# Optimization experiments

Hardware: AMD Instinct MI355X
Metric: run time of the kernel (lower is better)

## Reference

```python
import jax, jax.numpy as jnp
import numpy as np

N, E, F, C, ED, G, D = 50000, 1000000, 30, 64, 11, 1024, 256


def setup_inputs() -> dict:
    key = jax.random.key(0)
    ks = jax.random.split(key, 20)
    rn = lambda k, shape, s=0.1: jax.random.normal(k, shape, jnp.float32) * s
    return {
        "x": rn(ks[0], (N, F), 1.0),
        "edge_attr": jax.random.uniform(ks[1], (E, ED), jnp.float32),
        "W0": rn(ks[2], (F, C)), "asrc0": rn(ks[3], (C,)), "adst0": rn(ks[4], (C,)),
        "We0": rn(ks[5], (ED, C)), "ae0": rn(ks[6], (C,)), "Wres0": rn(ks[7], (F, C)),
        "b0": jnp.zeros((C,), jnp.float32),
        "W": rn(ks[8], (3, C, C)), "asrc": rn(ks[9], (3, C)), "adst": rn(ks[10], (3, C)),
        "We": rn(ks[11], (3, ED, C)), "ae": rn(ks[12], (3, C)), "Wres": rn(ks[13], (3, C, C)),
        "b": jnp.zeros((3, C), jnp.float32),
        "Wout": rn(ks[14], (2 * C, D)), "bout": jnp.zeros((D,), jnp.float32),
        "edge_index": jax.random.randint(ks[15], (2, E), 0, N),
        "batch_index": jnp.sort(jax.random.randint(ks[16], (N,), 0, G)),
    }


def _gat(x, src, dst, edge_attr, W, asrc, adst, We, ae, Wres, b):
    """PyG GATConv (heads=1) with edge_dim and residual=True."""
    n = x.shape[0]
    h = x @ W                                   # [N, C]
    e = edge_attr @ We                          # [E, C]
    alpha = (jnp.sum(h * asrc, -1)[src]
             + jnp.sum(h * adst, -1)[dst]
             + jnp.sum(e * ae, -1))             # [E]
    alpha = jax.nn.leaky_relu(alpha, 0.2)
    m = jax.ops.segment_max(alpha, dst, num_segments=n)
    a = jnp.exp(alpha - m[dst])
    s = jax.ops.segment_sum(a, dst, num_segments=n)
    a = a / (s[dst] + 1e-16)                    # per-dst softmax
    out = jax.ops.segment_sum(a[:, None] * h[src], dst, num_segments=n)
    return out + x @ Wres + b


def reference(x, edge_attr, W0, asrc0, adst0, We0, ae0, Wres0, b0,
              W, asrc, adst, We, ae, Wres, b, Wout, bout,
              edge_index, batch_index):
    src, dst = edge_index[0], edge_index[1]
    h = jax.nn.leaky_relu(
        _gat(x, src, dst, edge_attr, W0, asrc0, adst0, We0, ae0, Wres0, b0), 0.01)
    for i in range(3):  # conv1..conv3 (fixed small layer loop)
        h = _gat(h, src, dst, edge_attr, W[i], asrc[i], adst[i],
                 We[i], ae[i], Wres[i], b[i])
        if i < 2:
            h = jax.nn.leaky_relu(h, 0.01)
    gmax = jax.ops.segment_max(h, batch_index, num_segments=G)
    gmax = jnp.where(jnp.isfinite(gmax), gmax, 0.0)  # empty graphs -> 0
    cnt = jax.ops.segment_sum(jnp.ones((h.shape[0],), h.dtype), batch_index,
                              num_segments=G)
    gmean = jax.ops.segment_sum(h, batch_index, num_segments=G) / jnp.maximum(cnt, 1.0)[:, None]
    pooled = jax.nn.leaky_relu(jnp.concatenate([gmax, gmean], axis=1), 0.01)
    return pooled @ Wout + bout
```

## Files before the change

kernel.cpp:

```cpp
#include <hip/hip_runtime.h>
#include <hip/hip_fp16.h>

#define NN 50000
#define NE 1000000
#define FIN0 30
#define C 64
#define ED 11
#define NG 1024
#define DOUT 256
#define NBIN 196
#define PA_EDGES 2048

typedef unsigned long long ull;

__global__ __launch_bounds__(256) void hist196_kernel(const int* __restrict__ dst,
    int* __restrict__ bcnt){
  __shared__ int h[256];
  int t=threadIdx.x;
  h[t]=0;
  __syncthreads();
  for(int i=blockIdx.x*256+t;i<NE;i+=gridDim.x*256)
    atomicAdd(&h[dst[i]>>8],1);
  __syncthreads();
  if(h[t]) atomicAdd(&bcnt[t],h[t]);
}

__global__ __launch_bounds__(256) void scan196_kernel(const int* __restrict__ bcnt,
    int* __restrict__ bbase, int* __restrict__ gcur){
  __shared__ int p[256];
  int t=threadIdx.x;
  int v=bcnt[t];
  p[t]=v; __syncthreads();
  #pragma unroll
  for(int off=1;off<256;off<<=1){
    int u=(t>=off)?p[t-off]:0;
    __syncthreads(); p[t]+=u; __syncthreads();
  }
  int ex=p[t]-v;
  if(t<=NBIN) bbase[t]=ex;
  if(t<NBIN)  gcur[t]=ex;
}

__global__ __launch_bounds__(256) void grow_kernel(const int* __restrict__ batch,
    int* __restrict__ growptr){
  int i=blockIdx.x*256+threadIdx.x;
  if(i>=NN) return;
  int bi=batch[i];
  int bp=(i==0)?-1:batch[i-1];
  for(int g=bp+1;g<=bi;++g) growptr[g]=i;
  if(i==NN-1){ for(int g=bi+1;g<=NG;++g) growptr[g]=NN; }
}

__global__ __launch_bounds__(256) void part_kernel(const int* __restrict__ dst,
    const int* __restrict__ src, const float* __restrict__ edge_attr,
    const float* __restrict__ We0, const float* __restrict__ ae0,
    const float* __restrict__ We,  const float* __restrict__ ae,
    int* __restrict__ gcur, uint4* __restrict__ prec){
  __shared__ uint4 lrec[PA_EDGES];
  __shared__ unsigned char lbin[PA_EDGES];
  __shared__ float tile[256*ED];
  __shared__ float sw[4][ED];
  __shared__ int hist[256], p[256], sc[256], lofs[256], bb[256];
  int t=threadIdx.x;
  hist[t]=0;
  if(t<4*ED){
    int l=t/ED, j=t%ED;
    const float* wp=(l==0)? (We0+(size_t)j*C) : (We+((size_t)(l-1)*ED+j)*C);
    const float* ap=(l==0)? ae0 : (ae+(size_t)(l-1)*C);
    float s=0.f;
    for(int c=0;c<C;++c) s+=wp[c]*ap[c];
    sw[l][j]=s;
  }
  __syncthreads();
  size_t e0=(size_t)blockIdx.x*PA_EDGES;
  int cnt=(int)min((size_t)PA_EDGES,(size_t)NE-e0);
  for(int i=t;i<cnt;i+=256) atomicAdd(&hist[dst[e0+i]>>8],1);
  __syncthreads();
  p[t]=hist[t]; __syncthreads();
  #pragma unroll
  for(int off=1;off<256;off<<=1){
    int u=(t>=off)?p[t-off]:0;
    __syncthreads(); p[t]+=u; __syncthreads();
  }
  sc[t]=p[t]-hist[t];
  lofs[t]=sc[t];
  bb[t]=(hist[t]>0)?atomicAdd(&gcur[t],hist[t]):0;
  __syncthreads();
  for(int base=0;base<cnt;base+=256){
    int ccnt=min(256,cnt-base);
    for(int i=t;i<ccnt*ED;i+=256) tile[i]=edge_attr[(e0+base)*ED+i];
    __syncthreads();
    if(t<ccnt){
      int i=base+t;
      int d=dst[e0+i], s=src[e0+i];
      int b=d>>8;
      float d0=0,d1=0,d2=0,d3=0;
      #pragma unroll
      for(int j=0;j<ED;++j){
        float ev=tile[t*ED+j];
        d0=fmaf(ev,sw[0][j],d0);
        d1=fmaf(ev,sw[1][j],d1);
        d2=fmaf(ev,sw[2][j],d2);
        d3=fmaf(ev,sw[3][j],d3);
      }
      uint4 r;
      r.x=(unsigned)d; r.y=(unsigned)s;
      r.z=(unsigned)__half_as_ushort(__float2half(d0))
         |((unsigned)__half_as_ushort(__float2half(d1))<<16);
      r.w=(unsigned)__half_as_ushort(__float2half(d2))
         |((unsigned)__half_as_ushort(__float2half(d3))<<16);
      int slot=atomicAdd(&lofs[b],1);
      lrec[slot]=r;
      lbin[slot]=(unsigned char)b;
    }
    __syncthreads();
  }
  for(int i=t;i<cnt;i+=256){
    int b=lbin[i];
    int g=bb[b]+i-sc[b];
    prec[g]=lrec[i];
  }
}

__global__ __launch_bounds__(256) void build_kernel(const uint4* __restrict__ prec,
    const int* __restrict__ bbase,
    int* __restrict__ rowptr, int* __restrict__ src_csr, ushort* __restrict__ edch){
  __shared__ int cnt[256], p[256], cur[256];
  int t=threadIdx.x, b=blockIdx.x;
  int n0=b<<8;
  cnt[t]=0;
  __syncthreads();
  int beg=bbase[b], endd=bbase[b+1];
  for(int j=beg+t;j<endd;j+=256)
    atomicAdd(&cnt[(int)prec[j].x-n0],1);
  __syncthreads();
  int v=cnt[t];
  p[t]=v; __syncthreads();
  #pragma unroll
  for(int off=1;off<256;off<<=1){
    int u=(t>=off)?p[t-off]:0;
    __syncthreads(); p[t]+=u; __syncthreads();
  }
  int ex=p[t]-v;
  cur[t]=beg+ex;
  if(n0+t<NN) rowptr[n0+t]=beg+ex;
  if(b==0&&t==0) rowptr[NN]=NE;
  __syncthreads();
  for(int j=beg+t;j<endd;j+=256){
    uint4 r=prec[j];
    int d=(int)r.x, s=(int)r.y;
    int pos=atomicAdd(&cur[d-n0],1);
    src_csr[pos]=s;
    edch[pos]                =(ushort)(r.z&0xffffu);
    edch[(size_t)NE+pos]     =(ushort)(r.z>>16);
    edch[2*(size_t)NE+pos]   =(ushort)(r.w&0xffffu);
    edch[3*(size_t)NE+pos]   =(ushort)(r.w>>16);
  }
}

template<int FIN, int SXS>
__global__ __launch_bounds__(256) void feat_kernel(const float* __restrict__ in,
    const float* __restrict__ W, const float* __restrict__ Wres,
    const float* __restrict__ bvec, const float* __restrict__ av_src,
    const float* __restrict__ av_dst,
    __half* __restrict__ hW16, float* __restrict__ outb,
    float* __restrict__ as_, float* __restrict__ ad_){
  __shared__ float sW[FIN*C], sR[FIN*C];
  __shared__ float sx[64*SXS];
  __shared__ float sb[C], ss[C], sd[C];
  int tid=threadIdx.x;
  if(tid<C){ sb[tid]=bvec[tid]; ss[tid]=av_src[tid]; sd[tid]=av_dst[tid]; }
  for(int i=tid;i<FIN*C;i+=256){ sW[i]=W[i]; sR[i]=Wres[i]; }
  int nbase=blockIdx.x*64;
  int nvalid=min(64,NN-nbase);
  if constexpr (FIN==64){
    const float4* in4=(const float4*)(in+(size_t)nbase*64);
    for(int i=tid;i<1024;i+=256){
      int n=i>>4, k=(i&15)*4;
      float4 v=(n<nvalid)?in4[i]:make_float4(0.f,0.f,0.f,0.f);
      *(float4*)&sx[n*SXS+k]=v;
    }
  } else {
    for(int i=tid;i<64*FIN;i+=256){
      int n=i/FIN, k=i-n*FIN;
      sx[n*SXS+k]=(n<nvalid)?in[(size_t)(nbase+n)*FIN+k]:0.f;
    }
  }
  __syncthreads();
  int w=tid>>6, lane=tid&63;
  int ng=lane>>4, cl=lane&15;
  int n0=w*16+ng*4;
  int c0=cl*4;
  float hw[4][4]={}, hr[4][4]={};
  const float* sxp=&sx[n0*SXS];
  #pragma unroll 2
  for(int k=0;k<FIN;k+=2){
    float4 wv0=*(const float4*)&sW[k*C+c0];
    float4 rv0=*(const float4*)&sR[k*C+c0];
    float4 wv1=*(const float4*)&sW[(k+1)*C+c0];
    float4 rv1=*(const float4*)&sR[(k+1)*C+c0];
    float2 x0=*(const float2*)&sxp[k];
    float2 x1=*(const float2*)&sxp[SXS+k];
    float2 x2=*(const float2*)&sxp[2*SXS+k];
    float2 x3=*(const float2*)&sxp[3*SXS+k];
    float xa[4]={x0.x,x1.x,x2.x,x3.x};
    float xb[4]={x0.y,x1.y,x2.y,x3.y};
    #pragma unroll
    for(int r=0;r<4;++r){
      hw[r][0]=fmaf(xa[r],wv0.x,hw[r][0]);
      hw[r][1]=fmaf(xa[r],wv0.y,hw[r][1]);
      hw[r][2]=fmaf(xa[r],wv0.z,hw[r][2]);
      hw[r][3]=fmaf(xa[r],wv0.w,hw[r][3]);
      hr[r][0]=fmaf(xa[r],rv0.x,hr[r][0]);
      hr[r][1]=fmaf(xa[r],rv0.y,hr[r][1]);
      hr[r][2]=fmaf(xa[r],rv0.z,hr[r][2]);
      hr[r][3]=fmaf(xa[r],rv0.w,hr[r][3]);
      hw[r][0]=fmaf(xb[r],wv1.x,hw[r][0]);
      hw[r][1]=fmaf(xb[r],wv1.y,hw[r][1]);
      hw[r][2]=fmaf(xb[r],wv1.z,hw[r][2]);
      hw[r][3]=fmaf(xb[r],wv1.w,hw[r][3]);
      hr[r][0]=fmaf(xb[r],rv1.x,hr[r][0]);
      hr[r][1]=fmaf(xb[r],rv1.y,hr[r][1]);
      hr[r][2]=fmaf(xb[r],rv1.z,hr[r][2]);
      hr[r][3]=fmaf(xb[r],rv1.w,hr[r][3]);
    }
  }
  float s0=ss[c0], s1=ss[c0+1], s2=ss[c0+2], s3=ss[c0+3];
  float d0=sd[c0], d1=sd[c0+1], d2=sd[c0+2], d3=sd[c0+3];
  float b0v=sb[c0], b1v=sb[c0+1], b2v=sb[c0+2], b3v=sb[c0+3];
  #pragma unroll
  for(int r=0;r<4;++r){
    int n=n0+r;
    float ps=hw[r][0]*s0+hw[r][1]*s1+hw[r][2]*s2+hw[r][3]*s3;
    float pd=hw[r][0]*d0+hw[r][1]*d1+hw[r][2]*d2+hw[r][3]*d3;
    #pragma unroll
    for(int off=1;off<16;off<<=1){ ps+=__shfl_xor(ps,off,64); pd+=__shfl_xor(pd,off,64); }
    if(n<nvalid){
      size_t gn=(size_t)(nbase+n);
      ushort4 hv;
      hv.x=__half_as_ushort(__float2half(hw[r][0]));
      hv.y=__half_as_ushort(__float2half(hw[r][1]));
      hv.z=__half_as_ushort(__float2half(hw[r][2]));
      hv.w=__half_as_ushort(__float2half(hw[r][3]));
      *(ushort4*)&hW16[gn*C+c0]=hv;
      float4 ov;
      ov.x=hr[r][0]+b0v; ov.y=hr[r][1]+b1v; ov.z=hr[r][2]+b2v; ov.w=hr[r][3]+b3v;
      *(float4*)&outb[gn*C+c0]=ov;
      if(cl==0){ as_[gn]=ps; ad_[gn]=pd; }
    }
  }
}

__device__ __forceinline__ void acc8(float* a, float at, uint4 u){
  __half2 h0=*(__half2*)&u.x, h1=*(__half2*)&u.y, h2=*(__half2*)&u.z, h3=*(__half2*)&u.w;
  float2 f0=__half22float2(h0), f1=__half22float2(h1);
  float2 f2=__half22float2(h2), f3=__half22float2(h3);
  a[0]=fmaf(at,f0.x,a[0]); a[1]=fmaf(at,f0.y,a[1]);
  a[2]=fmaf(at,f1.x,a[2]); a[3]=fmaf(at,f1.y,a[3]);
  a[4]=fmaf(at,f2.x,a[4]); a[5]=fmaf(at,f2.y,a[5]);
  a[6]=fmaf(at,f3.x,a[6]); a[7]=fmaf(at,f3.y,a[7]);
}

__global__ __launch_bounds__(256) void agg_kernel(const int* __restrict__ rowptr,
    const int* __restrict__ src_csr, const ushort* __restrict__ edc_l,
    const float* __restrict__ as_, const float* __restrict__ ad_,
    const __half* __restrict__ hW16, float* __restrict__ outb, int relu){
  __shared__ float2 sws[4][64];
  int w=threadIdx.x>>6, lane=threadIdx.x&63;
  int half=lane>>5, hl=lane&31;
  int n0=blockIdx.x*8+w*2;
  int nidx=n0+half;
  int beg=rowptr[nidx], end=rowptr[nidx+1];
  int deg=end-beg;
  const uint4* hw4=(const uint4*)hW16;

  if(__all(deg<=32)){
    float ad_n=ad_[nidx];
    int j=beg+hl;
    float al=-INFINITY; int sl=0;
    if(hl<deg){
      sl=src_csr[j];
      float a=as_[sl]+ad_n+__half2float(__ushort_as_half(edc_l[j]));
      al=(a>0.f)?a:0.2f*a;
    }
    float mn=al;
    #pragma unroll
    for(int off=16;off;off>>=1) mn=fmaxf(mn,__shfl_xor(mn,off,64));
    float wl=(hl<deg)?__expf(al-mn):0.f;
    float s=wl;
    #pragma unroll
    for(int off=16;off;off>>=1) s+=__shfl_xor(s,off,64);
    float2 pr; pr.x=wl; pr.y=__int_as_float(sl);
    sws[w][lane]=pr;
    int g=hl>>3, gl=hl&7;
    float acc[8]={0.f,0.f,0.f,0.f,0.f,0.f,0.f,0.f};
    int base=half*32;
    int t=g;
    for(; t+4<deg; t+=8){
      float2 r0=sws[w][base+t], r1=sws[w][base+t+4];
      uint4 u0=hw4[(size_t)__float_as_int(r0.y)*8+gl];
      uint4 u1=hw4[(size_t)__float_as_int(r1.y)*8+gl];
      acc8(acc,r0.x,u0);
      acc8(acc,r1.x,u1);
    }
    if(t<deg){
      float2 r=sws[w][base+t];
      uint4 u=hw4[(size_t)__float_as_int(r.y)*8+gl];
      acc8(acc,r.x,u);
    }
    #pragma unroll
    for(int off=8;off<=16;off<<=1){
      #pragma unroll
      for(int i=0;i<8;++i) acc[i]+=__shfl_xor(acc[i],off,64);
    }
    if(hl<8){
      float denom=s+1e-16f;
      size_t o0=(size_t)nidx*C+hl*8;
      float4 oa=*(float4*)&outb[o0];
      float4 ob=*(float4*)&outb[o0+4];
      float4 va,vb;
      va.x=acc[0]/denom+oa.x; va.y=acc[1]/denom+oa.y;
      va.z=acc[2]/denom+oa.z; va.w=acc[3]/denom+oa.w;
      vb.x=acc[4]/denom+ob.x; vb.y=acc[5]/denom+ob.y;
      vb.z=acc[6]/denom+ob.z; vb.w=acc[7]/denom+ob.w;
      if(relu){
        va.x=(va.x>0.f)?va.x:0.01f*va.x; va.y=(va.y>0.f)?va.y:0.01f*va.y;
        va.z=(va.z>0.f)?va.z:0.01f*va.z; va.w=(va.w>0.f)?va.w:0.01f*va.w;
        vb.x=(vb.x>0.f)?vb.x:0.01f*vb.x; vb.y=(vb.y>0.f)?vb.y:0.01f*vb.y;
        vb.z=(vb.z>0.f)?vb.z:0.01f*vb.z; vb.w=(vb.w>0.f)?vb.w:0.01f*vb.w;
      }
      *(float4*)&outb[o0]=va;
      *(float4*)&outb[o0+4]=vb;
    }
    return;
  }

  for(int h=0;h<2;++h){
    int m=n0+h;
    int bh=__shfl(beg,h*32,64);
    int dh=__shfl(deg,h*32,64);
    float ad_n=ad_[m];
    int g2=lane>>3, gl2=lane&7;
    float s=0.f;
    float acc[8]={0.f,0.f,0.f,0.f,0.f,0.f,0.f,0.f};
    if(dh<=64){
      int j=bh+lane;
      float al=-INFINITY; int sl=0;
      if(lane<dh){
        sl=src_csr[j];
        float a=as_[sl]+ad_n+__half2float(__ushort_as_half(edc_l[j]));
        al=(a>0.f)?a:0.2f*a;
      }
      float mn=al;
      #pragma unroll
      for(int off=32;off;off>>=1) mn=fmaxf(mn,__shfl_xor(mn,off,64));
      float wl=(lane<dh)?__expf(al-mn):0.f;
      s=wl;
      #pragma unroll
      for(int off=32;off;off>>=1) s+=__shfl_xor(s,off,64);
      float2 pr; pr.x=wl; pr.y=__int_as_float(sl);
      sws[w][lane]=pr;
      int t=g2;
      for(; t+8<dh; t+=16){
        float2 r0=sws[w][t], r1=sws[w][t+8];
        uint4 u0=hw4[(size_t)__float_as_int(r0.y)*8+gl2];
        uint4 u1=hw4[(size_t)__float_as_int(r1.y)*8+gl2];
        acc8(acc,r0.x,u0);
        acc8(acc,r1.x,u1);
      }
      if(t<dh){
        float2 r=sws[w][t];
        uint4 u=hw4[(size_t)__float_as_int(r.y)*8+gl2];
        acc8(acc,r.x,u);
      }
    } else {
      float m_=-INFINITY;
      for(int base=bh;base<bh+dh;base+=64){
        int j=base+lane;
        float al=-INFINITY; int sl=0;
        if(j<bh+dh){
          sl=src_csr[j];
          float a=as_[sl]+ad_n+__half2float(__ushort_as_half(edc_l[j]));
          al=(a>0.f)?a:0.2f*a;
        }
        float cm=al;
        #pragma unroll
        for(int off=32;off;off>>=1) cm=fmaxf(cm,__shfl_xor(cm,off,64));
        float mn=fmaxf(m_,cm);
        float scale=(m_==-INFINITY)?0.f:__expf(m_-mn);
        s*=scale;
        #pragma unroll
        for(int i=0;i<8;++i) acc[i]*=scale;
        float wl=(j<bh+dh)?__expf(al-mn):0.f;
        float cs=wl;
        #pragma unroll
        for(int off=32;off;off>>=1) cs+=__shfl_xor(cs,off,64);
        s+=cs; m_=mn;
        float2 pr; pr.x=wl; pr.y=__int_as_float(sl);
        sws[w][lane]=pr;
        int cnt=min(64,bh+dh-base);
        int t=g2;
        for(; t+8<cnt; t+=16){
          float2 r0=sws[w][t], r1=sws[w][t+8];
          uint4 u0=hw4[(size_t)__float_as_int(r0.y)*8+gl2];
          uint4 u1=hw4[(size_t)__float_as_int(r1.y)*8+gl2];
          acc8(acc,r0.x,u0);
          acc8(acc,r1.x,u1);
        }
        if(t<cnt){
          float2 r=sws[w][t];
          uint4 u=hw4[(size_t)__float_as_int(r.y)*8+gl2];
          acc8(acc,r.x,u);
        }
      }
    }
    #pragma unroll
    for(int off=8;off<64;off<<=1){
      #pragma unroll
      for(int i=0;i<8;++i) acc[i]+=__shfl_xor(acc[i],off,64);
    }
    if(g2==0){
      float denom=s+1e-16f;
      size_t o0=(size_t)m*C+gl2*8;
      float4 oa=*(float4*)&outb[o0];
      float4 ob=*(float4*)&outb[o0+4];
      float4 va,vb;
      va.x=acc[0]/denom+oa.x; va.y=acc[1]/denom+oa.y;
      va.z=acc[2]/denom+oa.z; va.w=acc[3]/denom+oa.w;
      vb.x=acc[4]/denom+ob.x; vb.y=acc[5]/denom+ob.y;
      vb.z=acc[6]/denom+ob.z; vb.w=acc[7]/denom+ob.w;
      if(relu){
        va.x=(va.x>0.f)?va.x:0.01f*va.x; va.y=(va.y>0.f)?va.y:0.01f*va.y;
        va.z=(va.z>0.f)?va.z:0.01f*va.z; va.w=(va.w>0.f)?va.w:0.01f*va.w;
        vb.x=(vb.x>0.f)?vb.x:0.01f*vb.x; vb.y=(vb.y>0.f)?vb.y:0.01f*vb.y;
        vb.z=(vb.z>0.f)?vb.z:0.01f*vb.z; vb.w=(vb.w>0.f)?vb.w:0.01f*vb.w;
      }
      *(float4*)&outb[o0]=va;
      *(float4*)&outb[o0+4]=vb;
    }
  }
}

__global__ __launch_bounds__(256) void pool_kernel(const float* __restrict__ h,
    const int* __restrict__ growptr, float* __restrict__ pooled){
  int w=threadIdx.x>>6, lane=threadIdx.x&63;
  int g=blockIdx.x*4+w;
  if(g>=NG) return;
  int beg=growptr[g], end=growptr[g+1];
  float mx=-INFINITY, sm=0.f;
  for(int n=beg;n<end;++n){ float v=h[(size_t)n*C+lane]; mx=fmaxf(mx,v); sm+=v; }
  int cnt=end-beg;
  float gm=(cnt==0)?0.f:mx;
  float mean=sm/fmaxf((float)cnt,1.f);
  gm=(gm>0.f)?gm:0.01f*gm;
  mean=(mean>0.f)?mean:0.01f*mean;
  pooled[(size_t)g*128+lane]=gm;
  pooled[(size_t)g*128+64+lane]=mean;
}

__global__ __launch_bounds__(256) void out_kernel(const float* __restrict__ pooled,
    const float* __restrict__ Wout, const float* __restrict__ bout,
    float* __restrict__ out){
  __shared__ float sp[128];
  int g=blockIdx.x, d=threadIdx.x;
  if(d<128) sp[d]=pooled[(size_t)g*128+d];
  __syncthreads();
  float o=bout[d];
  for(int k=0;k<128;++k) o=fmaf(sp[k],Wout[k*DOUT+d],o);
  out[(size_t)g*DOUT+d]=o;
}

extern "C" void kernel_launch(void* const* d_in, const int* in_sizes, int n_in,
                              void* d_out, int out_size, void* d_ws, size_t ws_size,
                              hipStream_t stream){
  const float* x        =(const float*)d_in[0];
  const float* edge_attr=(const float*)d_in[1];
  const float* W0       =(const float*)d_in[2];
  const float* asrc0    =(const float*)d_in[3];
  const float* adst0    =(const float*)d_in[4];
  const float* We0      =(const float*)d_in[5];
  const float* ae0      =(const float*)d_in[6];
  const float* Wres0    =(const float*)d_in[7];
  const float* b0       =(const float*)d_in[8];
  const float* W        =(const float*)d_in[9];
  const float* asrc     =(const float*)d_in[10];
  const float* adst     =(const float*)d_in[11];
  const float* We       =(const float*)d_in[12];
  const float* ae       =(const float*)d_in[13];
  const float* Wres     =(const float*)d_in[14];
  const float* b        =(const float*)d_in[15];
  const float* Wout     =(const float*)d_in[16];
  const float* bout     =(const float*)d_in[17];
  const int* edge_index =(const int*)d_in[18];
  const int* batch_index=(const int*)d_in[19];
  const int* src=edge_index;
  const int* dst=edge_index+NE;

  char* p=(char*)d_ws;
  auto take=[&](size_t bytes)->void*{ void* r=(void*)p; p+=(bytes+255)&~(size_t)255; return r; };
  int* rowptr  =(int*)take((size_t)(NN+1)*4);
  int* growptr =(int*)take((size_t)(NG+1)*4);
  int* bcnt    =(int*)take((size_t)256*4);
  int* bbase   =(int*)take((size_t)256*4);
  int* gcur    =(int*)take((size_t)256*4);
  int* src_csr =(int*)take((size_t)NE*4);
  float* as_   =(float*)take((size_t)NN*4);
  float* ad_   =(float*)take((size_t)NN*4);
  ushort* edch =(ushort*)take((size_t)NE*4*2);
  __half* hW16 =(__half*)take((size_t)NN*C*2);
  float* bufA  =(float*)take((size_t)NN*C*4);
  uint4* prec  =(uint4*)take((size_t)NE*16);
  float* bufB  =(float*)prec;
  float* pooled=(float*)take((size_t)NG*128*4);
  (void)ws_size; (void)in_sizes; (void)n_in; (void)out_size;

  hipMemsetAsync(bcnt,0,(size_t)256*4,stream);
  hist196_kernel<<<1024,256,0,stream>>>(dst,bcnt);
  scan196_kernel<<<1,256,0,stream>>>(bcnt,bbase,gcur);
  grow_kernel<<<(NN+255)/256,256,0,stream>>>(batch_index,growptr);

  part_kernel<<<(NE+PA_EDGES-1)/PA_EDGES,256,0,stream>>>(dst,src,edge_attr,
      We0,ae0,We,ae,gcur,prec);
  build_kernel<<<NBIN,256,0,stream>>>(prec,bbase,rowptr,src_csr,edch);

  const int nblkF=(NN+63)/64;
  const int nblkA=NN/8;
  feat_kernel<FIN0,36><<<nblkF,256,0,stream>>>(x,W0,Wres0,b0,asrc0,adst0,hW16,bufA,as_,ad_);
  agg_kernel<<<nblkA,256,0,stream>>>(rowptr,src_csr,edch,as_,ad_,hW16,bufA,1);
  float* bin=bufA; float* bo=bufB;
  for(int i=0;i<3;++i){
    feat_kernel<C,68><<<nblkF,256,0,stream>>>(bin,W+(size_t)i*C*C,Wres+(size_t)i*C*C,
        b+(size_t)i*C,asrc+(size_t)i*C,adst+(size_t)i*C,hW16,bo,as_,ad_);
    agg_kernel<<<nblkA,256,0,stream>>>(rowptr,src_csr,edch+(size_t)(i+1)*NE,as_,ad_,hW16,bo,(i<2)?1:0);
    float* t=bin; bin=bo; bo=t;
  }
  pool_kernel<<<(NG+3)/4,256,0,stream>>>(bin,growptr,pooled);
  out_kernel<<<NG,256,0,stream>>>(pooled,Wout,bout,(float*)d_out);
}
```

Measured before the change: 312.5 us.

## Shrink partition tiles, use wave-shuffle scan, and drop shared staging buffers

```diff
diff --git a/kernel.cpp b/kernel.cpp
--- a/kernel.cpp
+++ b/kernel.cpp
@@ -9,7 +9,7 @@
 #define NG 1024
 #define DOUT 256
 #define NBIN 196
-#define PA_EDGES 2048
+#define PA_EDGES 1024
 
 typedef unsigned long long ull;
 
@@ -57,10 +57,9 @@
     const float* __restrict__ We,  const float* __restrict__ ae,
     int* __restrict__ gcur, uint4* __restrict__ prec){
   __shared__ uint4 lrec[PA_EDGES];
-  __shared__ unsigned char lbin[PA_EDGES];
-  __shared__ float tile[256*ED];
   __shared__ float sw[4][ED];
-  __shared__ int hist[256], p[256], sc[256], lofs[256], bb[256];
+  __shared__ int hist[256], sc[256], lofs[256], bb[256];
+  __shared__ int wsum[4];
   int t=threadIdx.x;
   hist[t]=0;
   if(t<4*ED){
@@ -74,51 +73,64 @@
   __syncthreads();
   size_t e0=(size_t)blockIdx.x*PA_EDGES;
   int cnt=(int)min((size_t)PA_EDGES,(size_t)NE-e0);
-  for(int i=t;i<cnt;i+=256) atomicAdd(&hist[dst[e0+i]>>8],1);
-  __syncthreads();
-  p[t]=hist[t]; __syncthreads();
-  #pragma unroll
-  for(int off=1;off<256;off<<=1){
-    int u=(t>=off)?p[t-off]:0;
-    __syncthreads(); p[t]+=u; __syncthreads();
-  }
-  sc[t]=p[t]-hist[t];
-  lofs[t]=sc[t];
-  bb[t]=(hist[t]>0)?atomicAdd(&gcur[t],hist[t]):0;
-  __syncthreads();
-  for(int base=0;base<cnt;base+=256){
-    int ccnt=min(256,cnt-base);
-    for(int i=t;i<ccnt*ED;i+=256) tile[i]=edge_attr[(e0+base)*ED+i];
-    __syncthreads();
-    if(t<ccnt){
-      int i=base+t;
-      int d=dst[e0+i], s=src[e0+i];
-      int b=d>>8;
+  int dreg[4], sreg[4];
+  #pragma unroll
+  for(int r=0;r<4;++r){
+    int i=r*256+t;
+    if(i<cnt){
+      dreg[r]=dst[e0+i]; sreg[r]=src[e0+i];
+      atomicAdd(&hist[dreg[r]>>8],1);
+    } else dreg[r]=-1;
+  }
+  __syncthreads();
+  int v=hist[t];
+  int inc=v;
+  #pragma unroll
+  for(int off=1;off<64;off<<=1){
+    int u=__shfl_up(inc,off,64);
+    if((t&63)>=off) inc+=u;
+  }
+  if((t&63)==63) wsum[t>>6]=inc;
+  __syncthreads();
+  int woff=0;
+  int myw=t>>6;
+  #pragma unroll
+  for(int k=0;k<3;++k) if(k<myw) woff+=wsum[k];
+  int ex=woff+inc-v;
+  sc[t]=ex;
+  lofs[t]=ex;
+  bb[t]=(v>0)?atomicAdd(&gcur[t],v):0;
+  __syncthreads();
+  #pragma unroll
+  for(int r=0;r<4;++r){
+    int i=r*256+t;
+    if(i<cnt){
+      const float* ea=edge_attr+(e0+i)*(size_t)ED;
       float d0=0,d1=0,d2=0,d3=0;
       #pragma unroll
       for(int j=0;j<ED;++j){
-        float ev=tile[t*ED+j];
+        float ev=ea[j];
         d0=fmaf(ev,sw[0][j],d0);
         d1=fmaf(ev,sw[1][j],d1);
         d2=fmaf(ev,sw[2][j],d2);
         d3=fmaf(ev,sw[3][j],d3);
       }
-      uint4 r;
-      r.x=(unsigned)d; r.y=(unsigned)s;
-      r.z=(unsigned)__half_as_ushort(__float2half(d0))
-         |((unsigned)__half_as_ushort(__float2half(d1))<<16);
-      r.w=(unsigned)__half_as_ushort(__float2half(d2))
-         |((unsigned)__half_as_ushort(__float2half(d3))<<16);
-      int slot=atomicAdd(&lofs[b],1);
-      lrec[slot]=r;
-      lbin[slot]=(unsigned char)b;
-    }
-    __syncthreads();
-  }
+      uint4 rec;
+      rec.x=(unsigned)dreg[r]; rec.y=(unsigned)sreg[r];
+      rec.z=(unsigned)__half_as_ushort(__float2half(d0))
+           |((unsigned)__half_as_ushort(__float2half(d1))<<16);
+      rec.w=(unsigned)__half_as_ushort(__float2half(d2))
+           |((unsigned)__half_as_ushort(__float2half(d3))<<16);
+      int slot=atomicAdd(&lofs[dreg[r]>>8],1);
+      lrec[slot]=rec;
+    }
+  }
+  __syncthreads();
   for(int i=t;i<cnt;i+=256){
-    int b=lbin[i];
+    uint4 rec=lrec[i];
+    int b=(int)(rec.x>>8);
     int g=bb[b]+i-sc[b];
-    prec[g]=lrec[i];
+    prec[g]=rec;
   }
 }
 
```

Result: no change. 307.7 us (-1.5%).
